# Kernel tuning notes

Hardware: AMD Instinct MI355X
Metric: run time of the kernel (lower is better)

The kernel has to match this reference:

```python
import jax, jax.numpy as jnp
import numpy as np
from jax import lax

NUM_STATES = 1024
NUM_OBS = 512
BATCH = 64
SEQ = 128


def setup_inputs() -> dict:
    key = jax.random.key(0)
    k1, k2, k3, k4 = jax.random.split(key, 4)
    value = jax.random.randint(k1, (BATCH, SEQ), 0, NUM_OBS)  # int observation ids
    prior_logits = jax.random.normal(k2, (NUM_STATES,), dtype=jnp.float32)
    trans_logits = jax.random.normal(k3, (NUM_STATES, NUM_STATES), dtype=jnp.float32)
    emission_logits = jax.random.normal(k4, (NUM_STATES, NUM_OBS), dtype=jnp.float32)
    return {"value": value, "prior_logits": prior_logits,
            "trans_logits": trans_logits, "emission_logits": emission_logits}


def reference(value, prior_logits, trans_logits, emission_logits):
    # Categorical(...).logits in torch is log-normalized: logits - logsumexp(logits)
    prior_ln = jax.nn.log_softmax(prior_logits)                 # [S]
    trans_ln = jax.nn.log_softmax(trans_logits, axis=-1)        # [S_from, S_to], row-normalized
    emis_ln = jax.nn.log_softmax(emission_logits, axis=-1)      # [S, V]
    transT = trans_ln.T                                         # [S_to, S_from]

    # Per-timestep emission log-likelihoods: emis_ln[:, value] -> [S, B, T] -> [T, B, S]
    e = jnp.transpose(emis_ln[:, value], (2, 1, 0))

    alpha0 = e[0] + prior_ln                                    # [B, S]

    def step(alpha, e_t):
        # alpha_new[b, j] = e_t[b, j] + logsumexp_i(transT[j, i] + alpha[b, i])
        a = e_t + jax.nn.logsumexp(transT[None, :, :] + alpha[:, None, :], axis=2)
        return a, None

    alpha_final, _ = lax.scan(step, alpha0, e[1:])
    return jax.nn.logsumexp(alpha_final, axis=1)                # [B]
```

## Files before the change

kernel.cpp:

```cpp
#include <hip/hip_runtime.h>
#include <hip/hip_bf16.h>


typedef __attribute__((ext_vector_type(8))) short short8;
typedef __attribute__((ext_vector_type(4))) float f32x4;

#define ALBUF_OFF 0x310000
#define DEEP_WS_NEED (ALBUF_OFF + 128 * 131072)

__device__ __forceinline__ float bf2f(short x) {
  unsigned u = ((unsigned)(unsigned short)x) << 16;
  return __builtin_bit_cast(float, u);
}
__device__ __forceinline__ short f2bf(float f) {
  unsigned u = __builtin_bit_cast(unsigned, f);
  u += 0x7fffu + ((u >> 16) & 1u);
  return (short)(u >> 16);
}
__device__ __forceinline__ float waveReduceMax(float v) {
  #pragma unroll
  for (int d = 1; d < 64; d <<= 1) v = fmaxf(v, __shfl_xor(v, d, 64));
  return v;
}
__device__ __forceinline__ float waveReduceSum(float v) {
  #pragma unroll
  for (int d = 1; d < 64; d <<= 1) v += __shfl_xor(v, d, 64);
  return v;
}

__device__ __forceinline__ void store_u32_coh(unsigned* p, unsigned v) {
  asm volatile("global_store_dword %0, %1, off sc0 sc1" :: "v"(p), "v"(v) : "memory");
}
__device__ __forceinline__ unsigned load_u32_coh(const unsigned* p) {
  unsigned r;
  asm volatile("global_load_dword %0, %1, off sc0 sc1\n\ts_waitcnt vmcnt(0)"
               : "=v"(r) : "v"(p) : "memory");
  return r;
}
__device__ __forceinline__ void store_short8_coh(short* p, short8 v) {
  asm volatile("global_store_dwordx4 %0, %1, off sc0 sc1" :: "v"(p), "v"(v) : "memory");
}


__global__ __launch_bounds__(256) void k_rowstat(const float* __restrict__ x,
                                                 float* __restrict__ rstat) {
  __shared__ float sm[8];
  const int row = blockIdx.x;
  const float* p = x + row * 1024;
  const int tid = threadIdx.x;
  float m = -1e30f;
  for (int i = tid; i < 1024; i += 256) m = fmaxf(m, p[i]);
  m = waveReduceMax(m);
  if ((tid & 63) == 0) sm[tid >> 6] = m;
  __syncthreads();
  m = fmaxf(fmaxf(sm[0], sm[1]), fmaxf(sm[2], sm[3]));
  float s = 0.f;
  for (int i = tid; i < 1024; i += 256) s += __expf(p[i] - m);
  s = waveReduceSum(s);
  if ((tid & 63) == 0) sm[4 + (tid >> 6)] = s;
  __syncthreads();
  if (tid == 0) {
    float tot = sm[4] + sm[5] + sm[6] + sm[7];
    rstat[row * 2] = m;
    rstat[row * 2 + 1] = 1.0f / tot;
  }
}

__global__ __launch_bounds__(256) void k_fillP(const float* __restrict__ trans,
                                               const float* __restrict__ rstat,
                                               short* __restrict__ P_frag) {
  __shared__ float st[512];
  const int w = blockIdx.x, tid = threadIdx.x;
  for (int kk = 0; kk < 32; ++kk) {
    for (int idx = tid; idx < 512; idx += 256) {
      int il = idx >> 4, jl = idx & 15;
      int i = kk * 32 + il, j = w * 16 + jl;
      float m = rstat[i * 2], invs = rstat[i * 2 + 1];
      st[idx] = __expf(trans[i * 1024 + j] - m) * invs;
    }
    __syncthreads();
    for (int idx = tid; idx < 512; idx += 256) {
      int lane = idx >> 3, e = idx & 7;
      int il = ((lane >> 4) & 3) * 8 + e, jl = lane & 15;
      P_frag[w * 16384 + kk * 512 + idx] = f2bf(st[il * 16 + jl]);
    }
    __syncthreads();
  }
}

__global__ __launch_bounds__(256) void k_emis(const float* __restrict__ x,
                                              short* __restrict__ o) {
  __shared__ float sm[8];
  const int row = blockIdx.x;
  const float* p = x + row * 512;
  const int tid = threadIdx.x;
  float m = -1e30f;
  for (int i = tid; i < 512; i += 256) m = fmaxf(m, p[i]);
  m = waveReduceMax(m);
  if ((tid & 63) == 0) sm[tid >> 6] = m;
  __syncthreads();
  m = fmaxf(fmaxf(sm[0], sm[1]), fmaxf(sm[2], sm[3]));
  float s = 0.f;
  for (int i = tid; i < 512; i += 256) s += __expf(p[i] - m);
  s = waveReduceSum(s);
  if ((tid & 63) == 0) sm[4 + (tid >> 6)] = s;
  __syncthreads();
  float invs = 512.0f / (sm[4] + sm[5] + sm[6] + sm[7]);
  for (int i = tid; i < 512; i += 256)
    o[i * 1024 + row] = f2bf(__expf(p[i] - m) * invs);
}

__global__ __launch_bounds__(256) void k_prior(const float* __restrict__ x,
                                               float* __restrict__ o) {
  __shared__ float sm[8];
  const int tid = threadIdx.x;
  float m = -1e30f;
  for (int i = tid; i < 1024; i += 256) m = fmaxf(m, x[i]);
  m = waveReduceMax(m);
  if ((tid & 63) == 0) sm[tid >> 6] = m;
  __syncthreads();
  m = fmaxf(fmaxf(sm[0], sm[1]), fmaxf(sm[2], sm[3]));
  float s = 0.f;
  for (int i = tid; i < 1024; i += 256) s += __expf(x[i] - m);
  s = waveReduceSum(s);
  if ((tid & 63) == 0) sm[4 + (tid >> 6)] = s;
  __syncthreads();
  float invs = 1.0f / (sm[4] + sm[5] + sm[6] + sm[7]);
  for (int i = tid; i < 1024; i += 256) o[i] = __expf(x[i] - m) * invs;
}


#define LAU(OFF) asm volatile("global_load_dwordx4 %0, %1, off offset:" #OFF " sc0 sc1" \
                              : "=v"(a[OFF / 64]) : "v"(ab) : "memory")

template <bool DEEP>
__global__ __launch_bounds__(256, 1) void hmm_main(
    const int* __restrict__ value, const float* __restrict__ prior_p,
    const short* __restrict__ P_frag, const short* __restrict__ emisT,
    short* __restrict__ albuf, unsigned int* __restrict__ flg,
    float* __restrict__ out) {
  __shared__ __align__(16) short p_lds[65536];
  __shared__ int v_lds[128 * 16];
  __shared__ __align__(16) short o_lds[16 * 80];

  const int bx = blockIdx.x;
  const int d = bx & 3;
  const int m = bx >> 2;
  const int tid = threadIdx.x;
  const int lane = tid & 63;
  const int wid = tid >> 6;
  const int jl = lane & 15;
  const int kg = lane >> 4;
  const int jcol = m * 64 + wid * 16 + jl;
  const int bloc0 = kg * 4;

  {
    const short8* src = (const short8*)P_frag + m * 8192;
    short8* dst = (short8*)p_lds;
    #pragma unroll
    for (int i = 0; i < 32; ++i) dst[tid + i * 256] = src[tid + i * 256];
  }
  for (int i = tid; i < 2048; i += 256) {
    int bl = i >> 7, tt = i & 127;
    v_lds[tt * 16 + bl] = value[(d * 16 + bl) * 128 + tt];
  }
  __syncthreads();

  {
    float pj = prior_p[jcol];
    #pragma unroll
    for (int r = 0; r < 4; ++r) {
      int obs = v_lds[bloc0 + r];
      float sv = pj * bf2f(emisT[obs * 1024 + jcol]);
      o_lds[(bloc0 + r) * 80 + wid * 16 + jl] = f2bf(sv);
    }
    __syncthreads();
    if (tid < 128) {
      int row = tid >> 3, chunk = tid & 7;
      short8 v = *(const short8*)(o_lds + row * 80 + chunk * 8);
      store_short8_coh(albuf + (size_t)(d * 16 + row) * 1024 + m * 64 + chunk * 8, v);
    }
    asm volatile("s_waitcnt vmcnt(0)" ::: "memory");
    __syncthreads();
    if (tid == 0) store_u32_coh(&flg[d * 2048 + 0 * 16 + m], 1u);
  }

  const short8* bb = (const short8*)p_lds + wid * 2048 + lane;

  float Ev[4];
  #pragma unroll
  for (int r = 0; r < 4; ++r)
    Ev[r] = bf2f(emisT[v_lds[1 * 16 + bloc0 + r] * 1024 + jcol]);

  for (int t = 1; t < 128; ++t) {
    if (wid == 0) {
      const unsigned* fp = flg + d * 2048 + (t - 1) * 16 + (lane & 15);
      int tries = 0;
      while (true) {
        unsigned f = load_u32_coh(fp);
        if (__all((int)(f == (unsigned)t))) break;
        if (++tries > (1 << 17)) break;
      }
    }
    __syncthreads();

    short8 a[32];
    f32x4 acc0 = {0.f, 0.f, 0.f, 0.f}, acc1 = {0.f, 0.f, 0.f, 0.f};
    if (DEEP) {
      const short8* ab8 = (const short8*)(albuf + (size_t)(t - 1) * 65536 +
                                          (d * 16 + jl) * 1024 + kg * 8);
      #pragma unroll
      for (int kk = 0; kk < 32; ++kk) a[kk] = ab8[kk * 4];
    } else {
      const void* ab = (const void*)(albuf + (size_t)((t - 1) & 1) * 65536 +
                                     (d * 16 + jl) * 1024 + kg * 8);
      LAU(0);    LAU(64);   LAU(128);  LAU(192);  LAU(256);  LAU(320);  LAU(384);  LAU(448);
      LAU(512);  LAU(576);  LAU(640);  LAU(704);  LAU(768);  LAU(832);  LAU(896);  LAU(960);
      LAU(1024); LAU(1088); LAU(1152); LAU(1216); LAU(1280); LAU(1344); LAU(1408); LAU(1472);
      LAU(1536); LAU(1600); LAU(1664); LAU(1728); LAU(1792); LAU(1856); LAU(1920); LAU(1984);
      asm volatile("s_waitcnt vmcnt(0)" ::: "memory");
      __builtin_amdgcn_sched_barrier(0);
    }

    #pragma unroll
    for (int kk = 0; kk < 32; kk += 2) {
      acc0 = __builtin_amdgcn_mfma_f32_16x16x32_bf16(a[kk], bb[kk * 64], acc0, 0, 0, 0);
      acc1 = __builtin_amdgcn_mfma_f32_16x16x32_bf16(a[kk + 1], bb[(kk + 1) * 64], acc1, 0, 0, 0);
    }

    #pragma unroll
    for (int r = 0; r < 4; ++r) {
      float sv = (acc0[r] + acc1[r]) * Ev[r];
      o_lds[(bloc0 + r) * 80 + wid * 16 + jl] = f2bf(sv);
    }
    __syncthreads();
    {
      size_t slot = DEEP ? (size_t)t : (size_t)(t & 1);
      if (tid < 128) {
        int row = tid >> 3, chunk = tid & 7;
        short8 v = *(const short8*)(o_lds + row * 80 + chunk * 8);
        store_short8_coh(albuf + slot * 65536 + (size_t)(d * 16 + row) * 1024 +
                         m * 64 + chunk * 8, v);
      }
      asm volatile("s_waitcnt vmcnt(0)" ::: "memory");
    }
    __syncthreads();
    if (tid == 0) store_u32_coh(&flg[d * 2048 + t * 16 + m], (unsigned)(t + 1));

    if (t < 127) {
      #pragma unroll
      for (int r = 0; r < 4; ++r)
        Ev[r] = bf2f(emisT[v_lds[(t + 1) * 16 + bloc0 + r] * 1024 + jcol]);
    }
  }

  if (m != 0) return;
  if (wid == 0) {
    const unsigned* fp = flg + d * 2048 + 127 * 16 + (lane & 15);
    int tries = 0;
    while (true) {
      unsigned f = load_u32_coh(fp);
      if (__all((int)(f == 128u))) break;
      if (++tries > (1 << 17)) break;
    }
  }
  __syncthreads();
  {
    size_t slot = DEEP ? (size_t)127 : (size_t)1;
    int row = tid >> 4, seg = tid & 15;
    const short8* base = (const short8*)(albuf + slot * 65536 +
                                         (size_t)(d * 16 + row) * 1024 + seg * 64);
    float s = 0.f;
    #pragma unroll
    for (int q = 0; q < 8; ++q) {
      short8 v = base[q];
      #pragma unroll
      for (int e = 0; e < 8; ++e) s += bf2f(v[e]);
    }
    #pragma unroll
    for (int msk = 1; msk < 16; msk <<= 1) s += __shfl_xor(s, msk, 64);
    if ((lane & 15) == 0) out[d * 16 + row] = logf(s) - 798.5055520050569f;
  }
}

extern "C" void kernel_launch(void* const* d_in, const int* in_sizes, int n_in,
                              void* d_out, int out_size, void* d_ws, size_t ws_size,
                              hipStream_t stream) {
  const int* value = (const int*)d_in[0];
  const float* prior = (const float*)d_in[1];
  const float* trans = (const float*)d_in[2];
  const float* emis = (const float*)d_in[3];
  char* ws = (char*)d_ws;
  short* P_frag = (short*)(ws + 0x000000);
  short* emisT = (short*)(ws + 0x200000);
  float* prior_p = (float*)(ws + 0x300000);
  float* rstat = (float*)(ws + 0x301000);
  unsigned* flg = (unsigned*)(ws + 0x303000);
  short* albuf = (short*)(ws + ALBUF_OFF);
  float* out = (float*)d_out;

  k_rowstat<<<1024, 256, 0, stream>>>(trans, rstat);
  k_fillP<<<64, 256, 0, stream>>>(trans, rstat, P_frag);
  k_emis<<<1024, 256, 0, stream>>>(emis, emisT);
  k_prior<<<1, 256, 0, stream>>>(prior, prior_p);
  if (ws_size >= (size_t)DEEP_WS_NEED) {
    hmm_main<true><<<64, 256, 0, stream>>>(value, prior_p, P_frag, emisT, albuf, flg, out);
  } else {
    hmm_main<false><<<64, 256, 0, stream>>>(value, prior_p, P_frag, emisT, albuf, flg, out);
  }
}
```

Before: 747.1 us.

## Replace flag-based cross-block sync with sentinel-polled data and register-resident transition tiles

In the deep path, the per-step flag handshake (spin on flags, then syncthreads, then a separate data load) is replaced. Each wave now polls the alpha buffer itself, which is pre-filled with a 0xAA sentinel by a memset, until no sign bit is set in the loaded words. The transition fragments move from LDS into registers, and the MFMA output is transposed so that each lane writes its 4 results directly with a single dwordx2 store, removing the LDS staging and the barriers. This trades a full-buffer memset and repeated 32-load polling traffic for a shorter inter-block critical path per timestep, and it relies on valid alpha values never having the sign bit set.

```diff
diff --git a/kernel.cpp b/kernel.cpp
--- a/kernel.cpp
+++ b/kernel.cpp
@@ -4,6 +4,9 @@
 
 typedef __attribute__((ext_vector_type(8))) short short8;
 typedef __attribute__((ext_vector_type(4))) float f32x4;
+typedef __attribute__((ext_vector_type(4))) float float4v;
+typedef __attribute__((ext_vector_type(4))) unsigned int uint4v;
+typedef __attribute__((ext_vector_type(2))) unsigned int uint2v;
 
 #define ALBUF_OFF 0x310000
 #define DEEP_WS_NEED (ALBUF_OFF + 128 * 131072)
@@ -27,7 +30,6 @@
   for (int d = 1; d < 64; d <<= 1) v += __shfl_xor(v, d, 64);
   return v;
 }
-
 __device__ __forceinline__ void store_u32_coh(unsigned* p, unsigned v) {
   asm volatile("global_store_dword %0, %1, off sc0 sc1" :: "v"(p), "v"(v) : "memory");
 }
@@ -36,9 +38,6 @@
   asm volatile("global_load_dword %0, %1, off sc0 sc1\n\ts_waitcnt vmcnt(0)"
                : "=v"(r) : "v"(p) : "memory");
   return r;
-}
-__device__ __forceinline__ void store_short8_coh(short* p, short8 v) {
-  asm volatile("global_store_dwordx4 %0, %1, off sc0 sc1" :: "v"(p), "v"(v) : "memory");
 }
 
 
@@ -130,8 +129,14 @@
 }
 
 
-#define LAU(OFF) asm volatile("global_load_dwordx4 %0, %1, off offset:" #OFF " sc0 sc1" \
-                              : "=v"(a[OFF / 64]) : "v"(ab) : "memory")
+#define PL(KK, OFF) asm volatile("global_load_dwordx4 %0, %1, off offset:" #OFF " sc0 sc1" \
+                                 : "=v"(u[KK]) : "v"(arow) : "memory")
+#define PL_ALL() do { \
+  PL(0,0);    PL(1,64);   PL(2,128);  PL(3,192);  PL(4,256);  PL(5,320);  PL(6,384);  PL(7,448); \
+  PL(8,512);  PL(9,576);  PL(10,640); PL(11,704); PL(12,768); PL(13,832); PL(14,896); PL(15,960); \
+  PL(16,1024);PL(17,1088);PL(18,1152);PL(19,1216);PL(20,1280);PL(21,1344);PL(22,1408);PL(23,1472); \
+  PL(24,1536);PL(25,1600);PL(26,1664);PL(27,1728);PL(28,1792);PL(29,1856);PL(30,1920);PL(31,1984); \
+} while (0)
 
 template <bool DEEP>
 __global__ __launch_bounds__(256, 1) void hmm_main(
@@ -139,9 +144,7 @@
     const short* __restrict__ P_frag, const short* __restrict__ emisT,
     short* __restrict__ albuf, unsigned int* __restrict__ flg,
     float* __restrict__ out) {
-  __shared__ __align__(16) short p_lds[65536];
-  __shared__ int v_lds[128 * 16];
-  __shared__ __align__(16) short o_lds[16 * 80];
+  __shared__ unsigned short v_lds[128 * 16];
 
   const int bx = blockIdx.x;
   const int d = bx & 3;
@@ -149,137 +152,159 @@
   const int tid = threadIdx.x;
   const int lane = tid & 63;
   const int wid = tid >> 6;
-  const int jl = lane & 15;
+  const int bl = lane & 15;
   const int kg = lane >> 4;
-  const int jcol = m * 64 + wid * 16 + jl;
-  const int bloc0 = kg * 4;
-
+  const int j0 = m * 64 + wid * 16 + kg * 4;
+
+  short8 pf[32];
   {
-    const short8* src = (const short8*)P_frag + m * 8192;
-    short8* dst = (short8*)p_lds;
+    const short8* pfsrc = (const short8*)(P_frag + (m * 4 + wid) * 16384) + lane;
     #pragma unroll
-    for (int i = 0; i < 32; ++i) dst[tid + i * 256] = src[tid + i * 256];
+    for (int kk = 0; kk < 32; ++kk) pf[kk] = pfsrc[kk * 64];
   }
   for (int i = tid; i < 2048; i += 256) {
-    int bl = i >> 7, tt = i & 127;
-    v_lds[tt * 16 + bl] = value[(d * 16 + bl) * 128 + tt];
+    int bli = i >> 7, tt = i & 127;
+    v_lds[tt * 16 + bli] = (unsigned short)value[(d * 16 + bli) * 128 + tt];
   }
   __syncthreads();
 
   {
-    float pj = prior_p[jcol];
-    #pragma unroll
-    for (int r = 0; r < 4; ++r) {
-      int obs = v_lds[bloc0 + r];
-      float sv = pj * bf2f(emisT[obs * 1024 + jcol]);
-      o_lds[(bloc0 + r) * 80 + wid * 16 + jl] = f2bf(sv);
-    }
-    __syncthreads();
-    if (tid < 128) {
-      int row = tid >> 3, chunk = tid & 7;
-      short8 v = *(const short8*)(o_lds + row * 80 + chunk * 8);
-      store_short8_coh(albuf + (size_t)(d * 16 + row) * 1024 + m * 64 + chunk * 8, v);
-    }
-    asm volatile("s_waitcnt vmcnt(0)" ::: "memory");
-    __syncthreads();
-    if (tid == 0) store_u32_coh(&flg[d * 2048 + 0 * 16 + m], 1u);
-  }
-
-  const short8* bb = (const short8*)p_lds + wid * 2048 + lane;
-
-  float Ev[4];
-  #pragma unroll
-  for (int r = 0; r < 4; ++r)
-    Ev[r] = bf2f(emisT[v_lds[1 * 16 + bloc0 + r] * 1024 + jcol]);
+    float4v pr = *(const float4v*)(prior_p + j0);
+    int obs = (int)v_lds[0 * 16 + bl];
+    uint2v e0 = *(const uint2v*)(emisT + obs * 1024 + j0);
+    float E0[4] = { bf2f((short)(e0.x & 0xffff)), bf2f((short)(e0.x >> 16)),
+                    bf2f((short)(e0.y & 0xffff)), bf2f((short)(e0.y >> 16)) };
+    unsigned b01 = ((unsigned)(unsigned short)f2bf(pr.x * E0[0])) |
+                   ((unsigned)(unsigned short)f2bf(pr.y * E0[1]) << 16);
+    unsigned b23 = ((unsigned)(unsigned short)f2bf(pr.z * E0[2])) |
+                   ((unsigned)(unsigned short)f2bf(pr.w * E0[3]) << 16);
+    uint2v ov = { b01, b23 };
+    short* wout = albuf + (size_t)(d * 16 + bl) * 1024 + j0;
+    asm volatile("global_store_dwordx2 %0, %1, off sc0 sc1" :: "v"(wout), "v"(ov) : "memory");
+    if (!DEEP) {
+      asm volatile("s_waitcnt vmcnt(0)" ::: "memory");
+      __syncthreads();
+      if (tid == 0) store_u32_coh(&flg[d * 2048 + 0 * 16 + m], 1u);
+    }
+  }
+
+  uint2v ef;
+  {
+    int obs = (int)v_lds[1 * 16 + bl];
+    ef = *(const uint2v*)(emisT + obs * 1024 + j0);
+  }
 
   for (int t = 1; t < 128; ++t) {
-    if (wid == 0) {
-      const unsigned* fp = flg + d * 2048 + (t - 1) * 16 + (lane & 15);
+    size_t slot_in = DEEP ? (size_t)(t - 1) : (size_t)((t - 1) & 1);
+    const short* arow = albuf + slot_in * 65536 + (size_t)(d * 16 + bl) * 1024 + kg * 8;
+    uint4v u[32];
+
+    if (DEEP) {
       int tries = 0;
       while (true) {
-        unsigned f = load_u32_coh(fp);
-        if (__all((int)(f == (unsigned)t))) break;
+        PL_ALL();
+        asm volatile("s_waitcnt vmcnt(0)" ::: "memory");
+        __builtin_amdgcn_sched_barrier(0);
+        unsigned bad = 0;
+        #pragma unroll
+        for (int kk = 0; kk < 32; ++kk) bad |= (u[kk].x | u[kk].z);
+        if (__all((int)((bad & 0x8000u) == 0u))) break;
         if (++tries > (1 << 17)) break;
       }
-    }
-    __syncthreads();
-
-    short8 a[32];
-    f32x4 acc0 = {0.f, 0.f, 0.f, 0.f}, acc1 = {0.f, 0.f, 0.f, 0.f};
-    if (DEEP) {
-      const short8* ab8 = (const short8*)(albuf + (size_t)(t - 1) * 65536 +
-                                          (d * 16 + jl) * 1024 + kg * 8);
-      #pragma unroll
-      for (int kk = 0; kk < 32; ++kk) a[kk] = ab8[kk * 4];
     } else {
-      const void* ab = (const void*)(albuf + (size_t)((t - 1) & 1) * 65536 +
-                                     (d * 16 + jl) * 1024 + kg * 8);
-      LAU(0);    LAU(64);   LAU(128);  LAU(192);  LAU(256);  LAU(320);  LAU(384);  LAU(448);
-      LAU(512);  LAU(576);  LAU(640);  LAU(704);  LAU(768);  LAU(832);  LAU(896);  LAU(960);
-      LAU(1024); LAU(1088); LAU(1152); LAU(1216); LAU(1280); LAU(1344); LAU(1408); LAU(1472);
-      LAU(1536); LAU(1600); LAU(1664); LAU(1728); LAU(1792); LAU(1856); LAU(1920); LAU(1984);
+      if (wid == 0) {
+        const unsigned* fp = flg + d * 2048 + (t - 1) * 16 + bl;
+        int tries = 0;
+        while (true) {
+          unsigned f = load_u32_coh(fp);
+          if (__all((int)(f == (unsigned)t))) break;
+          if (++tries > (1 << 17)) break;
+        }
+      }
+      __syncthreads();
+      PL_ALL();
       asm volatile("s_waitcnt vmcnt(0)" ::: "memory");
       __builtin_amdgcn_sched_barrier(0);
     }
 
+    f32x4 acc0 = {0.f, 0.f, 0.f, 0.f}, acc1 = {0.f, 0.f, 0.f, 0.f};
     #pragma unroll
     for (int kk = 0; kk < 32; kk += 2) {
-      acc0 = __builtin_amdgcn_mfma_f32_16x16x32_bf16(a[kk], bb[kk * 64], acc0, 0, 0, 0);
-      acc1 = __builtin_amdgcn_mfma_f32_16x16x32_bf16(a[kk + 1], bb[(kk + 1) * 64], acc1, 0, 0, 0);
-    }
-
-    #pragma unroll
-    for (int r = 0; r < 4; ++r) {
-      float sv = (acc0[r] + acc1[r]) * Ev[r];
-      o_lds[(bloc0 + r) * 80 + wid * 16 + jl] = f2bf(sv);
-    }
-    __syncthreads();
-    {
-      size_t slot = DEEP ? (size_t)t : (size_t)(t & 1);
-      if (tid < 128) {
-        int row = tid >> 3, chunk = tid & 7;
-        short8 v = *(const short8*)(o_lds + row * 80 + chunk * 8);
-        store_short8_coh(albuf + slot * 65536 + (size_t)(d * 16 + row) * 1024 +
-                         m * 64 + chunk * 8, v);
-      }
+      acc0 = __builtin_amdgcn_mfma_f32_16x16x32_bf16(
+          pf[kk], __builtin_bit_cast(short8, u[kk]), acc0, 0, 0, 0);
+      acc1 = __builtin_amdgcn_mfma_f32_16x16x32_bf16(
+          pf[kk + 1], __builtin_bit_cast(short8, u[kk + 1]), acc1, 0, 0, 0);
+    }
+
+    float E0 = bf2f((short)(ef.x & 0xffff)), E1 = bf2f((short)(ef.x >> 16));
+    float E2 = bf2f((short)(ef.y & 0xffff)), E3 = bf2f((short)(ef.y >> 16));
+    unsigned b01 = ((unsigned)(unsigned short)f2bf((acc0[0] + acc1[0]) * E0)) |
+                   ((unsigned)(unsigned short)f2bf((acc0[1] + acc1[1]) * E1) << 16);
+    unsigned b23 = ((unsigned)(unsigned short)f2bf((acc0[2] + acc1[2]) * E2)) |
+                   ((unsigned)(unsigned short)f2bf((acc0[3] + acc1[3]) * E3) << 16);
+    uint2v ov = { b01, b23 };
+    size_t slot_out = DEEP ? (size_t)t : (size_t)(t & 1);
+    short* wout = albuf + slot_out * 65536 + (size_t)(d * 16 + bl) * 1024 + j0;
+    asm volatile("global_store_dwordx2 %0, %1, off sc0 sc1" :: "v"(wout), "v"(ov) : "memory");
+
+    if (!DEEP) {
       asm volatile("s_waitcnt vmcnt(0)" ::: "memory");
-    }
-    __syncthreads();
-    if (tid == 0) store_u32_coh(&flg[d * 2048 + t * 16 + m], (unsigned)(t + 1));
+      __syncthreads();
+      if (tid == 0) store_u32_coh(&flg[d * 2048 + t * 16 + m], (unsigned)(t + 1));
+    }
 
     if (t < 127) {
-      #pragma unroll
-      for (int r = 0; r < 4; ++r)
-        Ev[r] = bf2f(emisT[v_lds[(t + 1) * 16 + bloc0 + r] * 1024 + jcol]);
+      int obs = (int)v_lds[(t + 1) * 16 + bl];
+      ef = *(const uint2v*)(emisT + obs * 1024 + j0);
     }
   }
 
   if (m != 0) return;
-  if (wid == 0) {
-    const unsigned* fp = flg + d * 2048 + 127 * 16 + (lane & 15);
-    int tries = 0;
-    while (true) {
-      unsigned f = load_u32_coh(fp);
-      if (__all((int)(f == 128u))) break;
-      if (++tries > (1 << 17)) break;
-    }
-  }
-  __syncthreads();
   {
-    size_t slot = DEEP ? (size_t)127 : (size_t)1;
-    int row = tid >> 4, seg = tid & 15;
-    const short8* base = (const short8*)(albuf + slot * 65536 +
-                                         (size_t)(d * 16 + row) * 1024 + seg * 64);
+    size_t slotF = DEEP ? (size_t)127 : (size_t)1;
+    const short* arow = albuf + slotF * 65536 + (size_t)(d * 16 + bl) * 1024 + kg * 8;
+    uint4v u[32];
+    if (DEEP) {
+      int tries = 0;
+      while (true) {
+        PL_ALL();
+        asm volatile("s_waitcnt vmcnt(0)" ::: "memory");
+        __builtin_amdgcn_sched_barrier(0);
+        unsigned bad = 0;
+        #pragma unroll
+        for (int kk = 0; kk < 32; ++kk) bad |= (u[kk].x | u[kk].z);
+        if (__all((int)((bad & 0x8000u) == 0u))) break;
+        if (++tries > (1 << 17)) break;
+      }
+    } else {
+      if (wid == 0) {
+        const unsigned* fp = flg + d * 2048 + 127 * 16 + bl;
+        int tries = 0;
+        while (true) {
+          unsigned f = load_u32_coh(fp);
+          if (__all((int)(f == 128u))) break;
+          if (++tries > (1 << 17)) break;
+        }
+      }
+      __syncthreads();
+      PL_ALL();
+      asm volatile("s_waitcnt vmcnt(0)" ::: "memory");
+      __builtin_amdgcn_sched_barrier(0);
+    }
     float s = 0.f;
     #pragma unroll
-    for (int q = 0; q < 8; ++q) {
-      short8 v = base[q];
+    for (int kk = 0; kk < 32; ++kk) {
       #pragma unroll
-      for (int e = 0; e < 8; ++e) s += bf2f(v[e]);
-    }
-    #pragma unroll
-    for (int msk = 1; msk < 16; msk <<= 1) s += __shfl_xor(s, msk, 64);
-    if ((lane & 15) == 0) out[d * 16 + row] = logf(s) - 798.5055520050569f;
+      for (int q = 0; q < 4; ++q) {
+        unsigned w = (q == 0) ? u[kk].x : (q == 1) ? u[kk].y : (q == 2) ? u[kk].z : u[kk].w;
+        s += bf2f((short)(w & 0xffff));
+        s += bf2f((short)(w >> 16));
+      }
+    }
+    s += __shfl_xor(s, 16, 64);
+    s += __shfl_xor(s, 32, 64);
+    if (wid == 0 && lane < 16)
+      out[d * 16 + lane] = logf(s) - 798.5055520050569f;
   }
 }
 
@@ -304,6 +329,7 @@
   k_emis<<<1024, 256, 0, stream>>>(emis, emisT);
   k_prior<<<1, 256, 0, stream>>>(prior, prior_p);
   if (ws_size >= (size_t)DEEP_WS_NEED) {
+    hipMemsetAsync(albuf, 0xAA, 128 * 131072, stream);
     hmm_main<true><<<64, 256, 0, stream>>>(value, prior_p, P_frag, emisT, albuf, flg, out);
   } else {
     hmm_main<false><<<64, 256, 0, stream>>>(value, prior_p, P_frag, emisT, albuf, flg, out);
```

New measurement: 1.024 ms. 37.1% more time.
